# Performance work log

Measured on AMD Instinct MI355X. Metric: run time of the kernel, lower is better.

Reference implementation:

```python
import jax, jax.numpy as jnp
import numpy as np

N, E, T, H, D_IN, D_OUT = 50000, 320000, 4, 4, 128, 128
NEG_SLOPE = 0.2
LN_EPS = 1e-5


def setup_inputs() -> dict:
    key = jax.random.key(0)
    ks = jax.random.split(key, 10)
    x = jax.random.normal(ks[0], (N, D_IN), jnp.float32)
    edge_index = jax.random.randint(ks[1], (2, E), 0, N, jnp.int32)
    edge_attr = jax.random.randint(ks[2], (E,), 0, T, jnp.int32)
    W_gat = jax.random.normal(ks[3], (T, D_IN, H * D_OUT), jnp.float32) / np.sqrt(D_IN)
    a_src = jax.random.normal(ks[4], (T, H, D_OUT), jnp.float32) / np.sqrt(D_OUT)
    a_dst = jax.random.normal(ks[5], (T, H, D_OUT), jnp.float32) / np.sqrt(D_OUT)
    b_gat = jnp.zeros((T, D_OUT), jnp.float32)
    edge_type_weights = jnp.ones((T,), jnp.float32) / T
    W_fuse = jax.random.normal(ks[6], (T * D_OUT, D_OUT), jnp.float32) / np.sqrt(T * D_OUT)
    b_fuse = jnp.zeros((D_OUT,), jnp.float32)
    ln_gamma = jnp.ones((D_OUT,), jnp.float32)
    ln_beta = jnp.zeros((D_OUT,), jnp.float32)
    return {"x": x, "edge_index": edge_index, "edge_attr": edge_attr,
            "W_gat": W_gat, "a_src": a_src, "a_dst": a_dst, "b_gat": b_gat,
            "edge_type_weights": edge_type_weights, "W_fuse": W_fuse,
            "b_fuse": b_fuse, "ln_gamma": ln_gamma, "ln_beta": ln_beta}


def _gat_one_type(x, src_all, dst_all, mask_all, W, a_s, a_d, b):
    # x: [N, D_in]; src_all/dst_all: [E+N] (type-mask + self-loops on all nodes)
    n = x.shape[0]
    h = (x @ W).reshape(n, H, D_OUT)                      # [N, H, D]
    alpha_s = jnp.sum(h * a_s, axis=-1)                   # [N, H]
    alpha_d = jnp.sum(h * a_d, axis=-1)                   # [N, H]
    logit = jax.nn.leaky_relu(alpha_s[src_all] + alpha_d[dst_all], NEG_SLOPE)  # [Ea, H]
    neg_inf = jnp.float32(-1e30)
    logit = jnp.where(mask_all[:, None], logit, neg_inf)
    m = jax.ops.segment_max(logit, dst_all, num_segments=n)   # [N, H] (self-loops ensure finite)
    ex = jnp.exp(logit - m[dst_all])
    ex = jnp.where(mask_all[:, None], ex, 0.0)
    denom = jax.ops.segment_sum(ex, dst_all, num_segments=n)  # [N, H]
    alpha = ex / denom[dst_all]                                # [Ea, H]
    msg = alpha[:, :, None] * h[src_all]                       # [Ea, H, D]
    out = jax.ops.segment_sum(msg, dst_all, num_segments=n)   # [N, H, D]
    return out.mean(axis=1) + b                                # concat=False -> head mean


def reference(x, edge_index, edge_attr, W_gat, a_src, a_dst, b_gat,
              edge_type_weights, W_fuse, b_fuse, ln_gamma, ln_beta):
    n = x.shape[0]
    self_idx = jnp.arange(n, dtype=edge_index.dtype)
    src_all = jnp.concatenate([edge_index[0], self_idx])
    dst_all = jnp.concatenate([edge_index[1], self_idx])
    outs = []
    for t in range(T):
        mask_all = jnp.concatenate([edge_attr == t, jnp.ones((n,), bool)])
        outs.append(_gat_one_type(x, src_all, dst_all, mask_all,
                                  W_gat[t], a_src[t], a_dst[t], b_gat[t]))
    w = jax.nn.softmax(edge_type_weights)
    x_cat = jnp.concatenate([outs[t] * w[t] for t in range(T)], axis=1)  # [N, T*D]
    y = x_cat @ W_fuse + b_fuse
    mu = jnp.mean(y, axis=-1, keepdims=True)
    var = jnp.var(y, axis=-1, keepdims=True)
    y = (y - mu) / jnp.sqrt(var + LN_EPS) * ln_gamma + ln_beta
    return jax.nn.relu(y)
```

## Files before the change

### kernel.cpp

```cpp
#include <hip/hip_runtime.h>
#include <hip/hip_bf16.h>

#define TT 4
#define HH 4
#define DD 128
#define KAGG 2048

typedef __attribute__((ext_vector_type(8))) short short8;
typedef __attribute__((ext_vector_type(4))) float f32x4;
typedef __attribute__((ext_vector_type(4))) unsigned int uint4v;

__device__ __forceinline__ float lrelu(float z) { return z > 0.f ? z : 0.2f * z; }
__device__ __forceinline__ float bf2f(unsigned short u) {
  union { unsigned int i; float f; } v; v.i = ((unsigned int)u) << 16; return v.f;
}
__device__ __forceinline__ unsigned short f2b(float f) {
  union { float f; unsigned int i; } u; u.f = f;
  unsigned int r = u.i + 0x7fff + ((u.i >> 16) & 1);
  return (unsigned short)(r >> 16);
}
__device__ __forceinline__ void unpack8v(uint4v u, float* hv) {
  hv[0] = bf2f((unsigned short)(u.x & 0xffff));
  hv[1] = bf2f((unsigned short)(u.x >> 16));
  hv[2] = bf2f((unsigned short)(u.y & 0xffff));
  hv[3] = bf2f((unsigned short)(u.y >> 16));
  hv[4] = bf2f((unsigned short)(u.z & 0xffff));
  hv[5] = bf2f((unsigned short)(u.z >> 16));
  hv[6] = bf2f((unsigned short)(u.w & 0xffff));
  hv[7] = bf2f((unsigned short)(u.w >> 16));
}

__global__ __launch_bounds__(256) void prologue_kernel(
    const float* __restrict__ x, unsigned short* __restrict__ xb, int total4,
    const float* __restrict__ Wg, const float* __restrict__ a_s,
    const float* __restrict__ a_d, const float* __restrict__ W_fuse,
    const float* __restrict__ b_gat, const float* __restrict__ etw,
    const float* __restrict__ b_fuse, unsigned short* __restrict__ Gfrag,
    unsigned short* __restrict__ Pall, float* __restrict__ cbias,
    const int* __restrict__ dst, const int* __restrict__ attr,
    int* __restrict__ deg, int E, int N) {
  int bid = blockIdx.x;
  const int nconv = (total4 + 255) >> 8;
  if (bid < nconv) {
    int i = bid * 256 + threadIdx.x;
    if (i < total4) {
      float4 v = ((const float4*)x)[i];
      ushort4 o;
      o.x = f2b(v.x); o.y = f2b(v.y); o.z = f2b(v.z); o.w = f2b(v.w);
      ((ushort4*)xb)[i] = o;
    }
    return;
  }
  bid -= nconv;
  if (bid < 1041) {
    float e0 = etw[0], e1 = etw[1], e2 = etw[2], e3 = etw[3];
    float mx = fmaxf(fmaxf(e0, e1), fmaxf(e2, e3));
    float w0 = __expf(e0 - mx), w1 = __expf(e1 - mx), w2 = __expf(e2 - mx),
          w3 = __expf(e3 - mx);
    float inv = 1.f / (w0 + w1 + w2 + w3);
    float wts[4] = {w0 * inv, w1 * inv, w2 * inv, w3 * inv};
    if (bid < 1024) {
      int idx = bid * 256 + threadIdx.x;
      int f = idx >> 9, l = (idx >> 3) & 63, j = idx & 7;
      int kt = f >> 5, kk = (f >> 3) & 3, n = f & 7;
      int K = kt * 128 + kk * 32 + (l >> 4) * 8 + j;
      int col = n * 16 + (l & 15);
      int t = K >> 9, head = (K >> 7) & 3, k = K & 127;
      const float* wr = Wg + (size_t)t * 65536 + k * 512 + head * 128;
      const float* wf = W_fuse + (size_t)t * 128 * 128 + col;
      float s = 0.f;
      for (int m = 0; m < 128; ++m) s += wr[m] * wf[(size_t)m * 128];
      Gfrag[idx] = f2b(0.25f * wts[t] * s);
    } else if (bid < 1040) {
      int idx = (bid - 1024) * 256 + threadIdx.x;
      int c = idx >> 7, k = idx & 127;
      int t = c >> 3, jj = c & 7, head = jj & 3;
      const float* av = ((jj < 4) ? a_s : a_d) + (t * 4 + head) * 128;
      const float* wr = Wg + (size_t)t * 65536 + k * 512 + head * 128;
      float s = 0.f;
      for (int m = 0; m < 128; ++m) s += wr[m] * av[m];
      Pall[c * 128 + k] = f2b(s);
    } else {
      int j = threadIdx.x;
      if (j < 128) {
        float s = b_fuse[j];
        for (int t = 0; t < 4; ++t) {
          float st = 0.f;
          for (int m = 0; m < 128; ++m)
            st += b_gat[t * 128 + m] * W_fuse[(size_t)(t * 128 + m) * 128 + j];
          s += wts[t] * st;
        }
        cbias[j] = s;
      }
    }
    return;
  }
  bid -= 1041;
  int e = bid * 256 + threadIdx.x;
  if (e < E) atomicAdd(&deg[attr[e] * N + dst[e]], 1);
}

__global__ __launch_bounds__(1024) void scanfused_kernel(
    const int* __restrict__ deg, int* __restrict__ rowptr,
    int* __restrict__ cursor, int* __restrict__ gcur, int M) {
  __shared__ int sh[1024];
  __shared__ int base;
  int i = blockIdx.x * 1024 + threadIdx.x;
  int v = (i < M) ? deg[i] : 0;
  sh[threadIdx.x] = v;
  __syncthreads();
  for (int off = 1; off < 1024; off <<= 1) {
    int xx = (threadIdx.x >= off) ? sh[threadIdx.x - off] : 0;
    __syncthreads();
    sh[threadIdx.x] += xx;
    __syncthreads();
  }
  if (threadIdx.x == 1023) base = atomicAdd(gcur, sh[1023]);
  __syncthreads();
  if (i < M) {
    int r = base + sh[threadIdx.x] - v;
    rowptr[i] = r;
    cursor[i] = r;
  }
}

__global__ __launch_bounds__(256) void scatter_alpha_kernel(
    const int* __restrict__ src, const int* __restrict__ dst,
    const int* __restrict__ attr, int* __restrict__ cursor,
    int* __restrict__ slist, const unsigned short* __restrict__ xb,
    const unsigned short* __restrict__ Pall, float* __restrict__ as_,
    float* __restrict__ ad_, int E, int N) {
  __shared__ uint4 ldsv[2048];
  int bid = blockIdx.x;
  const int nsc = (E + 255) >> 8;
  if (bid < nsc) {
    int e = bid * 256 + threadIdx.x;
    if (e < E) {
      int p = atomicAdd(&cursor[attr[e] * N + dst[e]], 1);
      slist[p] = src[e];
    }
    return;
  }
  bid -= nsc;
  unsigned char* lds = (unsigned char*)ldsv;
  const int n0 = bid * 128;
  const int tid = threadIdx.x, lane = tid & 63, wid = tid >> 6;
  const int lr = lane & 15, lg = lane >> 4;
#pragma unroll
  for (int i = 0; i < 8; ++i) {
    int chunk = tid + i * 256;
    int row = chunk >> 4, k16 = chunk & 15;
    int gr = n0 + row;
    uint4 v = make_uint4(0, 0, 0, 0);
    if (gr < N) v = *(const uint4*)(xb + (size_t)gr * DD + k16 * 8);
    *(uint4*)(lds + ((row * 256 + k16 * 16) ^ ((row & 7) << 4))) = v;
  }
  __syncthreads();
  f32x4 acc[2][2] = {};
#pragma unroll
  for (int kk = 0; kk < 4; ++kk) {
    short8 a[2], b[2];
#pragma unroll
    for (int m = 0; m < 2; ++m) {
      int row = wid * 32 + m * 16 + lr;
      a[m] = *(const short8*)(lds + ((row * 256 + kk * 64 + (lg << 4)) ^ ((row & 7) << 4)));
    }
#pragma unroll
    for (int n = 0; n < 2; ++n) {
      int c = n * 16 + lr;
      b[n] = *(const short8*)(Pall + c * DD + kk * 32 + lg * 8);
    }
#pragma unroll
    for (int m = 0; m < 2; ++m)
#pragma unroll
      for (int n = 0; n < 2; ++n)
        acc[m][n] = __builtin_amdgcn_mfma_f32_16x16x32_bf16(a[m], b[n], acc[m][n], 0, 0, 0);
  }
#pragma unroll
  for (int m = 0; m < 2; ++m)
#pragma unroll
    for (int n = 0; n < 2; ++n) {
      int c = n * 16 + lr;
      int t = c >> 3, jj = c & 7, head = jj & 3;
      float* dstp = (jj & 4) ? ad_ : as_;
#pragma unroll
      for (int r = 0; r < 4; ++r) {
        int gr = n0 + wid * 32 + m * 16 + lg * 4 + r;
        if (gr < N) dstp[((size_t)t * N + gr) * 4 + head] = acc[m][n][r];
      }
    }
}

__global__ __launch_bounds__(256) void gather_kernel(
    const int* __restrict__ slist, const int* __restrict__ rowptr,
    const int* __restrict__ deg, const float* __restrict__ as_,
    const float* __restrict__ ad_, const unsigned short* __restrict__ xb,
    unsigned short* __restrict__ AGG, int N) {
  int t = blockIdx.y;
  int d = blockIdx.x * 4 + (threadIdx.x >> 6);
  if (d >= N) return;
  int lane = threadIdx.x & 63;
  int head = lane >> 4;
  int dofs = (lane & 15) * 8;
  size_t tn = (size_t)t * N;
  uint4v* outp = (uint4v*)(AGG + (size_t)d * KAGG + t * 512 + lane * 8);

  int base = rowptr[tn + d], dg = deg[tn + d];
  if (dg == 0) {
    uint4v u = *(const uint4v*)(xb + (size_t)d * DD + dofs);
    __builtin_nontemporal_store(u, outp);
    return;
  }

  float adh = ad_[(tn + d) * 4 + head];
  float es = __expf(lrelu(as_[(tn + d) * 4 + head] + adh));
  float den = es;
  float acc8[8], hv[8];
  unpack8v(*(const uint4v*)(xb + (size_t)d * DD + dofs), hv);
#pragma unroll
  for (int j = 0; j < 8; ++j) acc8[j] = es * hv[j];

  int i = 0;
  for (; i + 1 < dg; i += 2) {
    int s0 = slist[base + i], s1 = slist[base + i + 1];
    float av0 = as_[(tn + s0) * 4 + head];
    float av1 = as_[(tn + s1) * 4 + head];
    uint4v u0 = *(const uint4v*)(xb + (size_t)s0 * DD + dofs);
    uint4v u1 = *(const uint4v*)(xb + (size_t)s1 * DD + dofs);
    float q0 = __expf(lrelu(av0 + adh));
    float q1 = __expf(lrelu(av1 + adh));
    den += q0 + q1;
    unpack8v(u0, hv);
#pragma unroll
    for (int j = 0; j < 8; ++j) acc8[j] += q0 * hv[j];
    unpack8v(u1, hv);
#pragma unroll
    for (int j = 0; j < 8; ++j) acc8[j] += q1 * hv[j];
  }
  if (i < dg) {
    int s = slist[base + i];
    float av = as_[(tn + s) * 4 + head];
    uint4v u = *(const uint4v*)(xb + (size_t)s * DD + dofs);
    float q = __expf(lrelu(av + adh));
    den += q;
    unpack8v(u, hv);
#pragma unroll
    for (int j = 0; j < 8; ++j) acc8[j] += q * hv[j];
  }

  float r = 1.f / den;
  uint4v o;
  o.x = (unsigned)f2b(acc8[0] * r) | ((unsigned)f2b(acc8[1] * r) << 16);
  o.y = (unsigned)f2b(acc8[2] * r) | ((unsigned)f2b(acc8[3] * r) << 16);
  o.z = (unsigned)f2b(acc8[4] * r) | ((unsigned)f2b(acc8[5] * r) << 16);
  o.w = (unsigned)f2b(acc8[6] * r) | ((unsigned)f2b(acc8[7] * r) << 16);
  __builtin_nontemporal_store(o, outp);
}

__global__ __launch_bounds__(256) void gemmln_kernel(
    const unsigned short* __restrict__ AGG, const unsigned short* __restrict__ Gfrag,
    const float* __restrict__ cbias, const float* __restrict__ gamma,
    const float* __restrict__ beta, float* __restrict__ out, int N) {
  __shared__ uint4 bbuf[2][2048];
  const int n0 = blockIdx.x * 128;
  const int tid = threadIdx.x, lane = tid & 63, wid = tid >> 6;
  const int lr = lane & 15, lg = lane >> 4;
  const int wrow = n0 + wid * 32;

  uint4 bn[8], ac[8];
  uint4v an[8];
#pragma unroll
  for (int i = 0; i < 8; ++i)
    bn[i] = *(const uint4*)(Gfrag + (size_t)(i * 256 + tid) * 8);
#pragma unroll
  for (int i = 0; i < 8; ++i) {
    int m = i >> 2, kk = i & 3;
    int gr = wrow + m * 16 + lr;
    an[i] = (uint4v){0, 0, 0, 0};
    if (gr < N)
      an[i] = __builtin_nontemporal_load(
          (const uint4v*)(AGG + (size_t)gr * KAGG + kk * 32 + lg * 8));
  }
#pragma unroll
  for (int i = 0; i < 8; ++i) bbuf[0][i * 256 + tid] = bn[i];
  __syncthreads();
#pragma unroll
  for (int i = 0; i < 8; ++i) ac[i] = *(uint4*)&an[i];

  f32x4 acc[2][8] = {};
  int cur = 0;
  for (int kt = 0; kt < 16; ++kt) {
    if (kt < 15) {
#pragma unroll
      for (int i = 0; i < 8; ++i)
        bn[i] = *(const uint4*)(Gfrag + (size_t)(kt + 1) * 16384 + (size_t)(i * 256 + tid) * 8);
#pragma unroll
      for (int i = 0; i < 8; ++i) {
        int m = i >> 2, kk = i & 3;
        int gr = wrow + m * 16 + lr;
        an[i] = (uint4v){0, 0, 0, 0};
        if (gr < N)
          an[i] = __builtin_nontemporal_load(
              (const uint4v*)(AGG + (size_t)gr * KAGG + (kt + 1) * 128 + kk * 32 + lg * 8));
      }
    }
    const unsigned char* lds = (const unsigned char*)bbuf[cur];
#pragma unroll
    for (int kk = 0; kk < 4; ++kk) {
      short8 a0 = *(const short8*)&ac[0 * 4 + kk];
      short8 a1 = *(const short8*)&ac[1 * 4 + kk];
#pragma unroll
      for (int n = 0; n < 8; ++n) {
        short8 b = *(const short8*)(lds + (kk * 8 + n) * 1024 + lane * 16);
        acc[0][n] = __builtin_amdgcn_mfma_f32_16x16x32_bf16(a0, b, acc[0][n], 0, 0, 0);
        acc[1][n] = __builtin_amdgcn_mfma_f32_16x16x32_bf16(a1, b, acc[1][n], 0, 0, 0);
      }
    }
    if (kt < 15) {
#pragma unroll
      for (int i = 0; i < 8; ++i) bbuf[cur ^ 1][i * 256 + tid] = bn[i];
      __syncthreads();
      cur ^= 1;
#pragma unroll
      for (int i = 0; i < 8; ++i) ac[i] = *(uint4*)&an[i];
    }
  }

  float cb[8], gm[8], bt[8];
#pragma unroll
  for (int n = 0; n < 8; ++n) {
    cb[n] = cbias[n * 16 + lr];
    gm[n] = gamma[n * 16 + lr];
    bt[n] = beta[n * 16 + lr];
  }
#pragma unroll
  for (int m = 0; m < 2; ++m)
#pragma unroll
    for (int rr = 0; rr < 4; ++rr) {
      float y[8];
      float s = 0.f, ss = 0.f;
#pragma unroll
      for (int n = 0; n < 8; ++n) {
        y[n] = acc[m][n][rr] + cb[n];
        s += y[n];
        ss += y[n] * y[n];
      }
#pragma unroll
      for (int mask = 1; mask <= 8; mask <<= 1) {
        s += __shfl_xor(s, mask);
        ss += __shfl_xor(ss, mask);
      }
      float mean = s * (1.f / 128.f);
      float var = ss * (1.f / 128.f) - mean * mean;
      float rstd = rsqrtf(var + 1e-5f);
      int gr = wrow + m * 16 + lg * 4 + rr;
      if (gr < N) {
#pragma unroll
        for (int n = 0; n < 8; ++n) {
          float v = (y[n] - mean) * rstd * gm[n] + bt[n];
          out[(size_t)gr * DD + n * 16 + lr] = fmaxf(0.f, v);
        }
      }
    }
}

extern "C" void kernel_launch(void* const* d_in, const int* in_sizes, int n_in,
                              void* d_out, int out_size, void* d_ws, size_t ws_size,
                              hipStream_t stream) {
  const float* x      = (const float*)d_in[0];
  const int*   ei     = (const int*)d_in[1];
  const int*   attr   = (const int*)d_in[2];
  const float* Wg     = (const float*)d_in[3];
  const float* a_src  = (const float*)d_in[4];
  const float* a_dst  = (const float*)d_in[5];
  const float* b_gat  = (const float*)d_in[6];
  const float* etw    = (const float*)d_in[7];
  const float* W_fuse = (const float*)d_in[8];
  const float* b_fuse = (const float*)d_in[9];
  const float* gamma  = (const float*)d_in[10];
  const float* beta   = (const float*)d_in[11];

  const int N = in_sizes[0] / DD;
  const int E = in_sizes[2];
  const int* src = ei;
  const int* dst = ei + E;
  const int M = TT * N;

  char* ws = (char*)d_ws;
  size_t off = 0;
  auto alloc = [&](size_t bytes) {
    void* p = ws + off;
    off += (bytes + 255) & ~(size_t)255;
    return p;
  };
  unsigned short* AGG   = (unsigned short*)alloc((size_t)N * KAGG * 2);
  unsigned short* xb    = (unsigned short*)alloc((size_t)N * DD * 2);
  unsigned short* Gfrag = (unsigned short*)alloc((size_t)512 * 512 * 2);
  unsigned short* Pall  = (unsigned short*)alloc((size_t)32 * DD * 2);
  float* cbias          = (float*)alloc(128 * sizeof(float));
  float* as_            = (float*)alloc((size_t)TT * N * 4 * sizeof(float));
  float* ad_            = (float*)alloc((size_t)TT * N * 4 * sizeof(float));
  int* deg              = (int*)alloc((size_t)(M + 1) * sizeof(int));
  int* rowptr           = (int*)alloc((size_t)M * sizeof(int));
  int* cursor           = (int*)alloc((size_t)M * sizeof(int));
  int* slist            = (int*)alloc((size_t)E * sizeof(int));

  hipMemsetAsync(deg, 0, (size_t)(M + 1) * sizeof(int), stream);

  int total4x = N * DD / 4;
  int nconv = (total4x + 255) / 256;
  int nhist = (E + 255) / 256;
  prologue_kernel<<<nconv + 1041 + nhist, 256, 0, stream>>>(
      x, xb, total4x, Wg, a_src, a_dst, W_fuse, b_gat, etw, b_fuse,
      Gfrag, Pall, cbias, dst, attr, deg, E, N);

  scanfused_kernel<<<(M + 1023) / 1024, 1024, 0, stream>>>(deg, rowptr, cursor,
                                                           deg + M, M);

  int nalpha = (N + 127) / 128;
  scatter_alpha_kernel<<<nhist + nalpha, 256, 0, stream>>>(
      src, dst, attr, cursor, slist, xb, Pall, as_, ad_, E, N);

  dim3 ggrid((N + 3) / 4, TT);
  gather_kernel<<<ggrid, 256, 0, stream>>>(slist, rowptr, deg, as_, ad_, xb, AGG, N);

  gemmln_kernel<<<(N + 127) / 128, 256, 0, stream>>>(AGG, Gfrag, cbias, gamma, beta,
                                                     (float*)d_out, N);
}
```

Before: 221.7 us.

## Process all heads per lane in gather to reuse neighbor row loads

Remaps the gather kernel so each 16-lane group handles one destination node and computes all four heads, loading each neighbor's feature chunk and attention scalars once instead of once per head group. This cuts redundant gather loads at the cost of 4x per-lane exp/FMA work, larger register usage, and divergence between nodes sharing a wave. It also replaces nontemporal loads/stores of the aggregate buffer with regular ones so it can stay cached between gather and GEMM.

```diff
diff --git a/kernel.cpp b/kernel.cpp
--- a/kernel.cpp
+++ b/kernel.cpp
@@ -197,64 +197,94 @@
     const float* __restrict__ ad_, const unsigned short* __restrict__ xb,
     unsigned short* __restrict__ AGG, int N) {
   int t = blockIdx.y;
-  int d = blockIdx.x * 4 + (threadIdx.x >> 6);
+  int lane = threadIdx.x & 63;
+  int u = lane >> 4, c16 = lane & 15;
+  int d = blockIdx.x * 16 + (threadIdx.x >> 6) * 4 + u;
   if (d >= N) return;
-  int lane = threadIdx.x & 63;
-  int head = lane >> 4;
-  int dofs = (lane & 15) * 8;
   size_t tn = (size_t)t * N;
-  uint4v* outp = (uint4v*)(AGG + (size_t)d * KAGG + t * 512 + lane * 8);
+  int dofs = c16 * 8;
+  unsigned short* outp = AGG + (size_t)d * KAGG + t * 512 + dofs;
 
   int base = rowptr[tn + d], dg = deg[tn + d];
+  uint4v uself = *(const uint4v*)(xb + (size_t)d * DD + dofs);
   if (dg == 0) {
-    uint4v u = *(const uint4v*)(xb + (size_t)d * DD + dofs);
-    __builtin_nontemporal_store(u, outp);
+#pragma unroll
+    for (int h = 0; h < 4; ++h) *(uint4v*)(outp + h * DD) = uself;
     return;
   }
 
-  float adh = ad_[(tn + d) * 4 + head];
-  float es = __expf(lrelu(as_[(tn + d) * 4 + head] + adh));
-  float den = es;
-  float acc8[8], hv[8];
-  unpack8v(*(const uint4v*)(xb + (size_t)d * DD + dofs), hv);
-#pragma unroll
-  for (int j = 0; j < 8; ++j) acc8[j] = es * hv[j];
+  float4 ad4 = *(const float4*)(ad_ + (tn + d) * 4);
+  float4 av = *(const float4*)(as_ + (tn + d) * 4);
+  float q[4], den[4], hv[8], acc[4][8];
+  q[0] = __expf(lrelu(av.x + ad4.x));
+  q[1] = __expf(lrelu(av.y + ad4.y));
+  q[2] = __expf(lrelu(av.z + ad4.z));
+  q[3] = __expf(lrelu(av.w + ad4.w));
+  unpack8v(uself, hv);
+#pragma unroll
+  for (int h = 0; h < 4; ++h) {
+    den[h] = q[h];
+#pragma unroll
+    for (int j = 0; j < 8; ++j) acc[h][j] = q[h] * hv[j];
+  }
 
   int i = 0;
   for (; i + 1 < dg; i += 2) {
     int s0 = slist[base + i], s1 = slist[base + i + 1];
-    float av0 = as_[(tn + s0) * 4 + head];
-    float av1 = as_[(tn + s1) * 4 + head];
+    float4 a0 = *(const float4*)(as_ + (tn + s0) * 4);
+    float4 a1 = *(const float4*)(as_ + (tn + s1) * 4);
     uint4v u0 = *(const uint4v*)(xb + (size_t)s0 * DD + dofs);
     uint4v u1 = *(const uint4v*)(xb + (size_t)s1 * DD + dofs);
-    float q0 = __expf(lrelu(av0 + adh));
-    float q1 = __expf(lrelu(av1 + adh));
-    den += q0 + q1;
+    float q0[4], q1[4];
+    q0[0] = __expf(lrelu(a0.x + ad4.x));
+    q0[1] = __expf(lrelu(a0.y + ad4.y));
+    q0[2] = __expf(lrelu(a0.z + ad4.z));
+    q0[3] = __expf(lrelu(a0.w + ad4.w));
+    q1[0] = __expf(lrelu(a1.x + ad4.x));
+    q1[1] = __expf(lrelu(a1.y + ad4.y));
+    q1[2] = __expf(lrelu(a1.z + ad4.z));
+    q1[3] = __expf(lrelu(a1.w + ad4.w));
+#pragma unroll
+    for (int h = 0; h < 4; ++h) den[h] += q0[h] + q1[h];
     unpack8v(u0, hv);
 #pragma unroll
-    for (int j = 0; j < 8; ++j) acc8[j] += q0 * hv[j];
+    for (int h = 0; h < 4; ++h)
+#pragma unroll
+      for (int j = 0; j < 8; ++j) acc[h][j] += q0[h] * hv[j];
     unpack8v(u1, hv);
 #pragma unroll
-    for (int j = 0; j < 8; ++j) acc8[j] += q1 * hv[j];
+    for (int h = 0; h < 4; ++h)
+#pragma unroll
+      for (int j = 0; j < 8; ++j) acc[h][j] += q1[h] * hv[j];
   }
   if (i < dg) {
     int s = slist[base + i];
-    float av = as_[(tn + s) * 4 + head];
-    uint4v u = *(const uint4v*)(xb + (size_t)s * DD + dofs);
-    float q = __expf(lrelu(av + adh));
-    den += q;
-    unpack8v(u, hv);
-#pragma unroll
-    for (int j = 0; j < 8; ++j) acc8[j] += q * hv[j];
-  }
-
-  float r = 1.f / den;
-  uint4v o;
-  o.x = (unsigned)f2b(acc8[0] * r) | ((unsigned)f2b(acc8[1] * r) << 16);
-  o.y = (unsigned)f2b(acc8[2] * r) | ((unsigned)f2b(acc8[3] * r) << 16);
-  o.z = (unsigned)f2b(acc8[4] * r) | ((unsigned)f2b(acc8[5] * r) << 16);
-  o.w = (unsigned)f2b(acc8[6] * r) | ((unsigned)f2b(acc8[7] * r) << 16);
-  __builtin_nontemporal_store(o, outp);
+    float4 a = *(const float4*)(as_ + (tn + s) * 4);
+    uint4v ue = *(const uint4v*)(xb + (size_t)s * DD + dofs);
+    float qe[4];
+    qe[0] = __expf(lrelu(a.x + ad4.x));
+    qe[1] = __expf(lrelu(a.y + ad4.y));
+    qe[2] = __expf(lrelu(a.z + ad4.z));
+    qe[3] = __expf(lrelu(a.w + ad4.w));
+#pragma unroll
+    for (int h = 0; h < 4; ++h) den[h] += qe[h];
+    unpack8v(ue, hv);
+#pragma unroll
+    for (int h = 0; h < 4; ++h)
+#pragma unroll
+      for (int j = 0; j < 8; ++j) acc[h][j] += qe[h] * hv[j];
+  }
+
+#pragma unroll
+  for (int h = 0; h < 4; ++h) {
+    float r = 1.f / den[h];
+    uint4v o;
+    o.x = (unsigned)f2b(acc[h][0] * r) | ((unsigned)f2b(acc[h][1] * r) << 16);
+    o.y = (unsigned)f2b(acc[h][2] * r) | ((unsigned)f2b(acc[h][3] * r) << 16);
+    o.z = (unsigned)f2b(acc[h][4] * r) | ((unsigned)f2b(acc[h][5] * r) << 16);
+    o.w = (unsigned)f2b(acc[h][6] * r) | ((unsigned)f2b(acc[h][7] * r) << 16);
+    *(uint4v*)(outp + h * DD) = o;
+  }
 }
 
 __global__ __launch_bounds__(256) void gemmln_kernel(
@@ -267,8 +297,7 @@
   const int lr = lane & 15, lg = lane >> 4;
   const int wrow = n0 + wid * 32;
 
-  uint4 bn[8], ac[8];
-  uint4v an[8];
+  uint4 bn[8], an[8], ac[8];
 #pragma unroll
   for (int i = 0; i < 8; ++i)
     bn[i] = *(const uint4*)(Gfrag + (size_t)(i * 256 + tid) * 8);
@@ -276,16 +305,14 @@
   for (int i = 0; i < 8; ++i) {
     int m = i >> 2, kk = i & 3;
     int gr = wrow + m * 16 + lr;
-    an[i] = (uint4v){0, 0, 0, 0};
-    if (gr < N)
-      an[i] = __builtin_nontemporal_load(
-          (const uint4v*)(AGG + (size_t)gr * KAGG + kk * 32 + lg * 8));
+    an[i] = make_uint4(0, 0, 0, 0);
+    if (gr < N) an[i] = *(const uint4*)(AGG + (size_t)gr * KAGG + kk * 32 + lg * 8);
   }
 #pragma unroll
   for (int i = 0; i < 8; ++i) bbuf[0][i * 256 + tid] = bn[i];
   __syncthreads();
 #pragma unroll
-  for (int i = 0; i < 8; ++i) ac[i] = *(uint4*)&an[i];
+  for (int i = 0; i < 8; ++i) ac[i] = an[i];
 
   f32x4 acc[2][8] = {};
   int cur = 0;
@@ -298,10 +325,9 @@
       for (int i = 0; i < 8; ++i) {
         int m = i >> 2, kk = i & 3;
         int gr = wrow + m * 16 + lr;
-        an[i] = (uint4v){0, 0, 0, 0};
+        an[i] = make_uint4(0, 0, 0, 0);
         if (gr < N)
-          an[i] = __builtin_nontemporal_load(
-              (const uint4v*)(AGG + (size_t)gr * KAGG + (kt + 1) * 128 + kk * 32 + lg * 8));
+          an[i] = *(const uint4*)(AGG + (size_t)gr * KAGG + (kt + 1) * 128 + kk * 32 + lg * 8);
       }
     }
     const unsigned char* lds = (const unsigned char*)bbuf[cur];
@@ -322,7 +348,7 @@
       __syncthreads();
       cur ^= 1;
 #pragma unroll
-      for (int i = 0; i < 8; ++i) ac[i] = *(uint4*)&an[i];
+      for (int i = 0; i < 8; ++i) ac[i] = an[i];
     }
   }
 
@@ -421,7 +447,7 @@
   scatter_alpha_kernel<<<nhist + nalpha, 256, 0, stream>>>(
       src, dst, attr, cursor, slist, xb, Pall, as_, ad_, E, N);
 
-  dim3 ggrid((N + 3) / 4, TT);
+  dim3 ggrid((N + 15) / 16, TT);
   gather_kernel<<<ggrid, 256, 0, stream>>>(slist, rowptr, deg, as_, ad_, xb, AGG, N);
 
   gemmln_kernel<<<(N + 127) / 128, 256, 0, stream>>>(AGG, Gfrag, cbias, gamma, beta,
```

Result: faster. 198.2 us (-10.6%).
